# Kernel optimization log

Measured on AMD Instinct MI355X. Metric: run time of the kernel, lower is better.

Reference implementation:

```python
import jax, jax.numpy as jnp
from jax import lax
import numpy as np


def _lstm_dir(xg, w_hh, h0, c0, reverse):
    # xg: [B, L, 4H] precomputed input-gate contributions (incl. bias)
    def step(carry, xt):
        h, c = carry
        g = xt + h @ w_hh.T  # [B, 4H]
        i, f, gg, o = jnp.split(g, 4, axis=-1)  # torch gate order i,f,g,o
        c = jax.nn.sigmoid(f) * c + jax.nn.sigmoid(i) * jnp.tanh(gg)
        h = jax.nn.sigmoid(o) * jnp.tanh(c)
        return (h, c), h
    xs = jnp.swapaxes(xg, 0, 1)  # [L, B, 4H]
    _, hs = lax.scan(step, (h0, c0), xs, reverse=reverse)
    return jnp.swapaxes(hs, 0, 1)  # [B, L, H]


def _bilstm(x, w_ih_f, w_hh_f, b_f, w_ih_b, w_hh_b, b_b, h0, c0):
    B = x.shape[0]
    H = w_hh_f.shape[1]
    h0f = jnp.broadcast_to(h0[0], (B, H))
    c0f = jnp.broadcast_to(c0[0], (B, H))
    h0b = jnp.broadcast_to(h0[1], (B, H))
    c0b = jnp.broadcast_to(c0[1], (B, H))
    xg_f = jnp.einsum('bld,gd->blg', x, w_ih_f) + b_f
    xg_b = jnp.einsum('bld,gd->blg', x, w_ih_b) + b_b
    hf = _lstm_dir(xg_f, w_hh_f, h0f, c0f, False)
    hb = _lstm_dir(xg_b, w_hh_b, h0b, c0b, True)
    return jnp.concatenate([hf, hb], axis=-1)  # [B, L, 2H]


def _stem_forward(existence, unit_hidden, w_ih_f, w_hh_f, b_f, w_ih_b, w_hh_b, b_b,
                  orient_w, orient_b, h0, c0):
    ex = existence[..., None]                                  # [B, L, 1] bool
    uh = unit_hidden * ex.astype(unit_hidden.dtype)
    L = uh.shape[1]
    units, orients, exs = [], [], []
    for length in range(L, 0, -1):
        hs = _bilstm(uh, w_ih_f, w_hh_f, b_f, w_ih_b, w_hh_b, b_b, h0, c0)
        o = jnp.einsum('blh,oh->blo', hs, orient_w) + orient_b  # [B, length, 1]
        units.append(uh)
        orients.append(o)
        exs.append(ex)
        if length == 1:
            break
        right = o > 0
        lw = right[:, :-1] & ex[:, :-1]          # left child oriented right
        rw = (~right[:, 1:]) & ex[:, 1:]         # right child oriented left
        ex = lw | rw
        uh = uh[:, :-1] * lw.astype(uh.dtype) + uh[:, 1:] * rw.astype(uh.dtype)
    units.reverse(); orients.reverse(); exs.reverse()
    return (jnp.concatenate(units, axis=1),
            jnp.concatenate(orients, axis=1),
            jnp.concatenate(exs, axis=1))


def setup_inputs() -> dict:
    key = jax.random.key(0)
    ks = jax.random.split(key, 12)
    B, L, D, H = 128, 64, 512, 256
    s = 0.05
    return {
        'existence': jnp.ones((B, L), dtype=bool),
        'unit_hidden': jax.random.normal(ks[0], (B, L, D), jnp.float32),
        'w_ih_f': jax.random.normal(ks[1], (4 * H, D), jnp.float32) * s,
        'w_hh_f': jax.random.normal(ks[2], (4 * H, H), jnp.float32) * s,
        'b_f': jax.random.normal(ks[3], (4 * H,), jnp.float32) * s,
        'w_ih_b': jax.random.normal(ks[4], (4 * H, D), jnp.float32) * s,
        'w_hh_b': jax.random.normal(ks[5], (4 * H, H), jnp.float32) * s,
        'b_b': jax.random.normal(ks[6], (4 * H,), jnp.float32) * s,
        'orient_w': jax.random.normal(ks[7], (1, 2 * H), jnp.float32) * s,
        'orient_b': jax.random.normal(ks[8], (1,), jnp.float32) * s,
        'h0': jax.random.normal(ks[9], (2, 1, H), jnp.float32),
        'c0': jax.random.normal(ks[10], (2, 1, H), jnp.float32),
    }


def reference(existence, unit_hidden, w_ih_f, w_hh_f, b_f, w_ih_b, w_hh_b, b_b,
              orient_w, orient_b, h0, c0):
    return _stem_forward(existence, unit_hidden, w_ih_f, w_hh_f, b_f,
                         w_ih_b, w_hh_b, b_b, orient_w, orient_b, h0, c0)
```

## Files before the change

### kernel.cpp

```cpp
#include <hip/hip_runtime.h>
#include <cmath>

#define B 128
#define L 64
#define D 512
#define H 256
#define G4 1024
#define TOTROWS 2080
#define NBLK 256
#define GF_PAD 16

typedef float fx4 __attribute__((ext_vector_type(4)));

__device__ __forceinline__ float sigf(float x) { return 1.0f / (1.0f + expf(-x)); }

__device__ __forceinline__ void stg_sc_f32(float* p, float v) {
    asm volatile("global_store_dword %0, %1, off sc0 sc1" :: "v"(p), "v"(v) : "memory");
}
__device__ __forceinline__ void stg_sc_f64(double* p, double v) {
    asm volatile("global_store_dwordx2 %0, %1, off sc0 sc1" :: "v"(p), "v"(v) : "memory");
}
__device__ __forceinline__ void stg_sc_f4(float* p, float4 v) {
    fx4 w = __builtin_bit_cast(fx4, v);
    asm volatile("global_store_dwordx4 %0, %1, off sc0 sc1" :: "v"(p), "v"(w) : "memory");
}
__device__ __forceinline__ void ld4x4_sc(const float* p, fx4& a, fx4& b, fx4& c, fx4& d) {
    asm volatile(
        "global_load_dwordx4 %0, %4, off sc0 sc1\n\t"
        "global_load_dwordx4 %1, %4, off offset:16 sc0 sc1\n\t"
        "global_load_dwordx4 %2, %4, off offset:32 sc0 sc1\n\t"
        "global_load_dwordx4 %3, %4, off offset:48 sc0 sc1\n\t"
        "s_waitcnt vmcnt(0)"
        : "=&v"(a), "=&v"(b), "=&v"(c), "=&v"(d)
        : "v"(p) : "memory");
}
__device__ __forceinline__ bool any_nan(fx4 v) {
    return (v[0] != v[0]) | (v[1] != v[1]) | (v[2] != v[2]) | (v[3] != v[3]);
}

__device__ __forceinline__ void st_flag(int* p, int v) {
    __hip_atomic_store(p, v, __ATOMIC_RELAXED, __HIP_MEMORY_SCOPE_AGENT);
}
__device__ __forceinline__ int ld_flag(const int* p) {
    return __hip_atomic_load(p, __ATOMIC_RELAXED, __HIP_MEMORY_SCOPE_AGENT);
}

__device__ __forceinline__ void grid_barrier2(int* dflag, int* dgen, int bid, int phase) {
    __syncthreads();
    if (threadIdx.x == 0) {
        asm volatile("s_waitcnt vmcnt(0)" ::: "memory");
        st_flag(dflag + bid * GF_PAD, phase);
    }
    if (bid == 0) {
        if (threadIdx.x < 64) {
#pragma unroll
            for (int i = 0; i < 4; i++)
                while (ld_flag(dflag + (threadIdx.x * 4 + i) * GF_PAD) < phase)
                    __builtin_amdgcn_s_sleep(1);
        }
        __syncthreads();
        if (threadIdx.x == 0) st_flag(dgen, phase);
    } else if (threadIdx.x == 0) {
        while (ld_flag(dgen) < phase) __builtin_amdgcn_s_sleep(1);
    }
    __builtin_amdgcn_fence(__ATOMIC_ACQUIRE, "agent");
    __syncthreads();
}

__global__ __launch_bounds__(256) void k_init(const int* __restrict__ ex_in,
                                              const float* __restrict__ uh_in,
                                              float* __restrict__ units,
                                              float* __restrict__ exdst,
                                              float* __restrict__ hst,
                                              int* __restrict__ flags) {
    int idx = blockIdx.x * 256 + threadIdx.x;
    if (idx < 8192) flags[idx] = 0;
    {
        float qn = __uint_as_float(0x7fc00000u);
        float4 q4; q4.x = qn; q4.y = qn; q4.z = qn; q4.w = qn;
        ((float4*)hst)[idx] = q4;
    }
    int bt = idx >> 7;
    int r  = idx & 127;
    float m = (ex_in[bt] != 0) ? 1.0f : 0.0f;
    const float4* src = (const float4*)uh_in;
    float4 v = src[idx];
    v.x *= m; v.y *= m; v.z *= m; v.w *= m;
    int b = bt >> 6, t = bt & 63;
    float4* dst = (float4*)units;
    dst[((size_t)b * TOTROWS + 2016 + t) * 128 + r] = v;
    if (r == 0) exdst[bt] = m;
}

__global__ __launch_bounds__(256) void k_wprep_ih(const float* __restrict__ wf,
                                                  const float* __restrict__ wb,
                                                  float* __restrict__ wt) {
    int o = blockIdx.x * 256 + threadIdx.x;
    int n = o & 1023;
    int k = (o >> 10) & 511;
    int d = o >> 19;
    const float* W = d ? wb : wf;
    wt[o] = W[n * 512 + k];
}

__global__ __launch_bounds__(256) void k_wprep_hh(const float* __restrict__ wf,
                                                  const float* __restrict__ wb,
                                                  float* __restrict__ wt) {
    int o = blockIdx.x * 256 + threadIdx.x;
    int c    = o & 3;
    int i4   = (o >> 2) & 3;
    int q    = (o >> 4) & 3;
    int lane = (o >> 6) & 255;
    int jg   = (o >> 14) & 15;
    int d    = o >> 18;
    int jj = lane & 15, kseg = lane >> 4;
    const float* W = d ? wb : wf;
    wt[o] = W[(q * 256 + jg * 16 + jj) * 256 + kseg * 16 + i4 * 4 + c];
}

__global__ __launch_bounds__(256) void k_xg(const float* __restrict__ units,
                                            const float* __restrict__ wihT,
                                            float* __restrict__ xg, int len, int offL) {
    __shared__ __align__(16) float As[32 * 132];
    __shared__ __align__(16) float Bs[32 * 132];
    int tid = threadIdx.x;
    int nt = blockIdx.x, mtb = blockIdx.y;
    int d = nt >> 3;
    int gbase = (nt & 7) * 128;
    int M = 128 * len;

    int arow = tid & 127, ahalf = tid >> 7;
    int agm = mtb * 128 + arow;
    const float* aptr = nullptr;
    if (agm < M) {
        int ab = agm / len, at = agm - ab * len;
        aptr = units + ((size_t)ab * TOTROWS + offL + at) * 512;
    }
    int bcol = (tid & 31) * 4, bkr = tid >> 5;
    int tm = tid >> 4, tn = tid & 15;

    float acc[8][8];
#pragma unroll
    for (int i = 0; i < 8; i++)
#pragma unroll
        for (int j = 0; j < 8; j++) acc[i][j] = 0.f;

    for (int k0 = 0; k0 < 512; k0 += 32) {
#pragma unroll
        for (int i4 = 0; i4 < 4; i4++) {
            float4 v;
            if (aptr) v = *(const float4*)&aptr[k0 + ahalf * 16 + i4 * 4];
            else { v.x = v.y = v.z = v.w = 0.f; }
            int kk = ahalf * 16 + i4 * 4;
            As[(kk + 0) * 132 + arow] = v.x;
            As[(kk + 1) * 132 + arow] = v.y;
            As[(kk + 2) * 132 + arow] = v.z;
            As[(kk + 3) * 132 + arow] = v.w;
        }
#pragma unroll
        for (int i = 0; i < 4; i++) {
            int kk = bkr * 4 + i;
            float4 v = *(const float4*)&wihT[((size_t)(d * 512 + k0 + kk)) * 1024 + gbase + bcol];
            *(float4*)&Bs[kk * 132 + bcol] = v;
        }
        __syncthreads();
#pragma unroll 4
        for (int k = 0; k < 32; k++) {
            float4 a0 = *(const float4*)&As[k * 132 + tm * 8];
            float4 a1 = *(const float4*)&As[k * 132 + tm * 8 + 4];
            float4 b0 = *(const float4*)&Bs[k * 132 + tn * 8];
            float4 b1 = *(const float4*)&Bs[k * 132 + tn * 8 + 4];
            float av[8] = {a0.x, a0.y, a0.z, a0.w, a1.x, a1.y, a1.z, a1.w};
            float bv[8] = {b0.x, b0.y, b0.z, b0.w, b1.x, b1.y, b1.z, b1.w};
#pragma unroll
            for (int i = 0; i < 8; i++)
#pragma unroll
                for (int j = 0; j < 8; j++) acc[i][j] = fmaf(av[i], bv[j], acc[i][j]);
        }
        __syncthreads();
    }
#pragma unroll
    for (int i = 0; i < 8; i++) {
        int gm = mtb * 128 + tm * 8 + i;
        if (gm < M) {
            int bb = gm / len, tt = gm - bb * len;
            float* Cp = xg + ((size_t)(d * B + bb) * L + tt) * G4 + gbase + tn * 8;
            float4 v0; v0.x = acc[i][0]; v0.y = acc[i][1]; v0.z = acc[i][2]; v0.w = acc[i][3];
            float4 v1; v1.x = acc[i][4]; v1.y = acc[i][5]; v1.z = acc[i][6]; v1.w = acc[i][7];
            *(float4*)&Cp[0] = v0;
            *(float4*)&Cp[4] = v1;
        }
    }
}

__global__ __launch_bounds__(256, 1) void k_persist(
        float* __restrict__ xg, const float* __restrict__ wtHH,
        const float* __restrict__ bias_f, const float* __restrict__ bias_b,
        const float* __restrict__ ow, const float* __restrict__ h0,
        const float* __restrict__ c0, float* __restrict__ hst,
        double* __restrict__ o_part, const float* __restrict__ ob,
        float* __restrict__ exb0, float* __restrict__ exb1,
        float* __restrict__ dec, float* __restrict__ units,
        float* __restrict__ out_or, float* __restrict__ out_ex,
        int* flags) {
    __shared__ __align__(16) float hs[256 * 16];
    __shared__ __align__(16) float pb[8 * 16 * 68];
    __shared__ float osh[68];
    __shared__ float dsh[64];
    __shared__ float dsh2[64];
    int tid = threadIdx.x;
    int bid = blockIdx.x;
    int jg = bid & 15, sgd = bid >> 4;
    int sg = sgd & 7, d = sgd >> 3;
    int b0 = sg * 16, j0 = jg * 16;
    const size_t HB = (size_t)2 * B * H;

    int* dflag = flags;
    int* dgen  = flags + 4096;
    int dph = 0;

    float4 wreg[16];
    {
        const float4* wp = (const float4*)(wtHH + ((size_t)(d * 16 + jg) * 256 + tid) * 64);
#pragma unroll
        for (int m = 0; m < 16; m++) wreg[m] = wp[m];
    }
    int bF = tid >> 4, jjF = tid & 15;
    int bG = b0 + bF, jG = j0 + jjF;
    const float* biasp = d ? bias_b : bias_f;
    float bias4[4] = { biasp[jG], biasp[256 + jG], biasp[512 + jG], biasp[768 + jG] };
    float owv = ow[d * H + jG];
    float c0v = c0[d * H + jG];
    int bS = tid & 15, kc = tid >> 4;
    int swz = (((bS >> 2) ^ (kc & 3)) << 2) + (bS & 3);
    float4 h0s[4];
#pragma unroll
    for (int i4 = 0; i4 < 4; i4++)
        h0s[i4] = *(const float4*)&h0[d * H + kc * 16 + i4 * 4];
    const float* hstb = hst + ((size_t)(d * B + b0 + bS)) * H + kc * 16;
    float*       hwr  = hst + ((size_t)(d * B + bG)) * H + jG;
    float c_reg = 0.f;

    for (int it = 0; it < 64; ++it) {
        int len = 64 - it;
        int offL = len * (len - 1) / 2;
        int n = len - 1;
        const float* exs = (it & 1) ? exb1 : exb0;
        float* exd = (it & 1) ? exb0 : exb1;

        for (int s = 0; s < len; ++s) {
            int t = d ? (n - s) : s;
            size_t xgo = (((size_t)(d * B + bG)) * L + t) * G4 + jG;
            float x0 = xg[xgo], x1 = xg[xgo + 256], x2 = xg[xgo + 512], x3 = xg[xgo + 768];
            if (s == 0) {
#pragma unroll
                for (int i4 = 0; i4 < 4; i4++) {
                    int kk = kc * 16 + i4 * 4;
                    hs[(kk + 0) * 16 + swz] = h0s[i4].x;
                    hs[(kk + 1) * 16 + swz] = h0s[i4].y;
                    hs[(kk + 2) * 16 + swz] = h0s[i4].z;
                    hs[(kk + 3) * 16 + swz] = h0s[i4].w;
                }
            } else {
                const float* hp = hstb + (size_t)(s - 1) * HB;
                fx4 v0, v1, v2, v3;
                do { ld4x4_sc(hp, v0, v1, v2, v3); }
                while (any_nan(v0) | any_nan(v1) | any_nan(v2) | any_nan(v3));
                float arr[16] = { v0[0], v0[1], v0[2], v0[3], v1[0], v1[1], v1[2], v1[3],
                                  v2[0], v2[1], v2[2], v2[3], v3[0], v3[1], v3[2], v3[3] };
#pragma unroll
                for (int i = 0; i < 16; i++)
                    hs[(kc * 16 + i) * 16 + swz] = arr[i];
            }
            __syncthreads();
            {
                int jj = tid & 15, kseg = tid >> 4;
                int ks3 = kseg & 3;
                float acc[4][16];
#pragma unroll
                for (int q = 0; q < 4; q++)
#pragma unroll
                    for (int u = 0; u < 16; u++) acc[q][u] = 0.f;
#pragma unroll
                for (int i4 = 0; i4 < 4; i4++) {
#pragma unroll
                    for (int c = 0; c < 4; c++) {
                        int k = (kseg << 4) + (i4 << 2) + c;
                        const float* hb = &hs[k << 4];
                        float4 hv[4];
#pragma unroll
                        for (int bq = 0; bq < 4; bq++)
                            hv[bq] = *(const float4*)&hb[((bq ^ ks3) << 2)];
#pragma unroll
                        for (int q = 0; q < 4; q++) {
                            float4 wv = wreg[q * 4 + i4];
                            float w = (c == 0) ? wv.x : (c == 1) ? wv.y : (c == 2) ? wv.z : wv.w;
#pragma unroll
                            for (int bq = 0; bq < 4; bq++) {
                                acc[q][bq * 4 + 0] = fmaf(hv[bq].x, w, acc[q][bq * 4 + 0]);
                                acc[q][bq * 4 + 1] = fmaf(hv[bq].y, w, acc[q][bq * 4 + 1]);
                                acc[q][bq * 4 + 2] = fmaf(hv[bq].z, w, acc[q][bq * 4 + 2]);
                                acc[q][bq * 4 + 3] = fmaf(hv[bq].w, w, acc[q][bq * 4 + 3]);
                            }
                        }
                    }
                }
#pragma unroll
                for (int q = 0; q < 4; q++)
#pragma unroll
                    for (int u = 0; u < 16; u++) acc[q][u] += __shfl_xor(acc[q][u], 32);
                if (!(tid & 32)) {
                    int slice = ((tid >> 6) << 1) | ((tid >> 4) & 1);
                    float* pbp = &pb[(slice * 16 + jj) * 68];
#pragma unroll
                    for (int bb = 0; bb < 16; bb++) {
                        float4 v; v.x = acc[0][bb]; v.y = acc[1][bb]; v.z = acc[2][bb]; v.w = acc[3][bb];
                        *(float4*)&pbp[bb * 4] = v;
                    }
                }
            }
            __syncthreads();
            {
                float g4[4] = {0.f, 0.f, 0.f, 0.f};
#pragma unroll
                for (int sl = 0; sl < 8; sl++) {
                    float4 pv = *(const float4*)&pb[(sl * 16 + jjF) * 68 + bF * 4];
                    g4[0] += pv.x; g4[1] += pv.y; g4[2] += pv.z; g4[3] += pv.w;
                }
                float g0 = x0 + bias4[0] + g4[0];
                float g1 = x1 + bias4[1] + g4[1];
                float g2 = x2 + bias4[2] + g4[2];
                float g3 = x3 + bias4[3] + g4[3];
                float c_old = (s == 0) ? c0v : c_reg;
                float ig = sigf(g0);
                float fg = sigf(g1);
                float gv = tanhf(g2);
                float og = sigf(g3);
                float c = fg * c_old + ig * gv;
                float h = og * tanhf(c);
                c_reg = c;
                stg_sc_f32(hwr + (size_t)s * HB, h);
                double contrib = (double)h * (double)owv;
#pragma unroll
                for (int off = 8; off > 0; off >>= 1) contrib += __shfl_xor(contrib, off, 16);
                if (jjF == 0) stg_sc_f64(&o_part[(((size_t)(d * 16 + jg)) * B + bG) * L + t], contrib);
            }
            __syncthreads();
        }
        ++dph; grid_barrier2(dflag, dgen, bid, dph);

        if (bid < 128) {
            int b = bid;
            float oval = 0.f, exval = 0.f;
            if (tid < len) {
                double sum = (double)ob[0];
#pragma unroll 4
                for (int i = 0; i < 32; i++) sum += o_part[((size_t)i * B + b) * L + tid];
                oval = (float)sum;
                osh[tid] = oval;
                exval = exs[b * L + tid];
                stg_sc_f32(out_or + (size_t)b * TOTROWS + offL + tid, oval);
                stg_sc_f32(out_ex + (size_t)b * TOTROWS + offL + tid, exval);
            }
            __syncthreads();
            if (tid < len - 1) {
                float on  = osh[tid + 1];
                float exn = exs[b * L + tid + 1];
                float lw = (oval > 0.f && exval != 0.f) ? 1.f : 0.f;
                float rw = (!(on > 0.f) && exn != 0.f) ? 1.f : 0.f;
                stg_sc_f32(dec + b * L + tid, lw + 2.f * rw);
                stg_sc_f32(exd + b * L + tid, ((lw + rw) > 0.f) ? 1.f : 0.f);
            }
        }
        ++dph; grid_barrier2(dflag, dgen, bid, dph);

        if (len > 1) {
            int bu = bid >> 1;
            int b2 = bid & 127;
            if (tid < n) dsh[tid]  = dec[bu * L + tid];
            if (tid < n) dsh2[tid] = dec[b2 * L + tid];
            __syncthreads();
            {
                int k = ((bid & 1) << 8) + tid;
                const float* src = units + ((size_t)bu * TOTROWS + offL) * D + k;
                float* dst = units + ((size_t)bu * TOTROWS + (offL - n)) * D + k;
                float cur = src[0];
                int tt = 0;
                while (tt < n) {
                    int m = (n - tt < 8) ? (n - tt) : 8;
                    float nx[8];
#pragma unroll
                    for (int i = 0; i < 8; i++) if (i < m) nx[i] = src[(size_t)(tt + i + 1) * D];
#pragma unroll
                    for (int i = 0; i < 8; i++) if (i < m) {
                        int dv = (int)dsh[tt + i];
                        stg_sc_f32(dst + (size_t)(tt + i) * D,
                                   (float)(dv & 1) * cur + (float)(dv >> 1) * nx[i]);
                        cur = nx[i];
                    }
                    tt += m;
                }
            }
            {
                int d2 = bid >> 7;
                float* base = xg + ((size_t)(d2 * B + b2) * L) * G4 + tid * 4;
                float4 cur = *(const float4*)base;
                int tt = 0;
                while (tt < n) {
                    int m = (n - tt < 8) ? (n - tt) : 8;
                    float4 nx[8];
#pragma unroll
                    for (int i = 0; i < 8; i++) if (i < m)
                        nx[i] = *(const float4*)(base + (size_t)(tt + i + 1) * G4);
#pragma unroll
                    for (int i = 0; i < 8; i++) if (i < m) {
                        int dv = (int)dsh2[tt + i];
                        float flw = (float)(dv & 1), frw = (float)(dv >> 1);
                        float4 o;
                        o.x = flw * cur.x + frw * nx[i].x;
                        o.y = flw * cur.y + frw * nx[i].y;
                        o.z = flw * cur.z + frw * nx[i].z;
                        o.w = flw * cur.w + frw * nx[i].w;
                        stg_sc_f4(base + (size_t)(tt + i) * G4, o);
                        cur = nx[i];
                    }
                    tt += m;
                }
            }
            {
                float qn = __uint_as_float(0x7fc00000u);
                for (int s2 = 0; s2 < n; ++s2)
                    stg_sc_f32(hwr + (size_t)s2 * HB, qn);
            }
            ++dph; grid_barrier2(dflag, dgen, bid, dph);
        }
    }
}

extern "C" void kernel_launch(void* const* d_in, const int* in_sizes, int n_in,
                              void* d_out, int out_size, void* d_ws, size_t ws_size,
                              hipStream_t stream) {
    const int*   ex_in   = (const int*)d_in[0];
    const float* uh_in   = (const float*)d_in[1];
    const float* w_ih_f  = (const float*)d_in[2];
    const float* w_hh_f  = (const float*)d_in[3];
    const float* b_f     = (const float*)d_in[4];
    const float* w_ih_b  = (const float*)d_in[5];
    const float* w_hh_b  = (const float*)d_in[6];
    const float* b_b     = (const float*)d_in[7];
    const float* orientw = (const float*)d_in[8];
    const float* orientb = (const float*)d_in[9];
    const float* h0      = (const float*)d_in[10];
    const float* c0      = (const float*)d_in[11];

    float* units  = (float*)d_out;
    float* out_or = units + (size_t)B * TOTROWS * D;
    float* out_ex = out_or + (size_t)B * TOTROWS;

    float* xg    = (float*)d_ws;
    float* wihT  = xg + (size_t)2 * B * L * G4;
    float* wtHH  = wihT + (size_t)1048576;
    float* hst   = wtHH + (size_t)524288;
    float* dec   = hst + (size_t)64 * 2 * B * H;
    float* exb0  = dec + B * L;
    float* exb1  = exb0 + B * L;
    double* opart = (double*)(exb1 + B * L);
    int*   flags = (int*)(opart + 262144);

    k_init<<<4096, 256, 0, stream>>>(ex_in, uh_in, units, exb0, hst, flags);
    k_wprep_ih<<<4096, 256, 0, stream>>>(w_ih_f, w_ih_b, wihT);
    k_wprep_hh<<<2048, 256, 0, stream>>>(w_hh_f, w_hh_b, wtHH);
    k_xg<<<dim3(16, 64), 256, 0, stream>>>(units, wihT, xg, 64, 2016);
    k_persist<<<NBLK, 256, 0, stream>>>(xg, wtHH, b_f, b_b, orientw, h0, c0,
                                        hst, opart, orientb,
                                        exb0, exb1, dec, units, out_or, out_ex, flags);
    (void)in_sizes; (void)n_in; (void)out_size; (void)ws_size;
}
```

Measured before the change: 12.90 ms.

## Replace NaN-sentinel polling of hidden state with per-group step counters

Blocks used to spin-reload the 64-byte h slice until it contained no NaNs, which required NaN-filling the whole hst buffer at init and re-poisoning it after every outer iteration. Each writer now publishes a monotonically increasing step tag per (batch row, column group) after a vmcnt wait, and readers poll that single int before loading h once. This removes the NaN init and re-poison stores but adds a full store drain and an extra flag store on every step.

```diff
diff --git a/kernel.cpp b/kernel.cpp
--- a/kernel.cpp
+++ b/kernel.cpp
@@ -23,6 +23,15 @@
 __device__ __forceinline__ void stg_sc_f4(float* p, float4 v) {
     fx4 w = __builtin_bit_cast(fx4, v);
     asm volatile("global_store_dwordx4 %0, %1, off sc0 sc1" :: "v"(p), "v"(w) : "memory");
+}
+__device__ __forceinline__ void stg_sc_u32(int* p, int v) {
+    asm volatile("global_store_dword %0, %1, off sc0 sc1" :: "v"(p), "v"(v) : "memory");
+}
+__device__ __forceinline__ int ld_sc_u32(const int* p) {
+    int v;
+    asm volatile("global_load_dword %0, %1, off sc0 sc1\n\ts_waitcnt vmcnt(0)"
+                 : "=v"(v) : "v"(p) : "memory");
+    return v;
 }
 __device__ __forceinline__ void ld4x4_sc(const float* p, fx4& a, fx4& b, fx4& c, fx4& d) {
     asm volatile(
@@ -34,9 +43,6 @@
         : "=&v"(a), "=&v"(b), "=&v"(c), "=&v"(d)
         : "v"(p) : "memory");
 }
-__device__ __forceinline__ bool any_nan(fx4 v) {
-    return (v[0] != v[0]) | (v[1] != v[1]) | (v[2] != v[2]) | (v[3] != v[3]);
-}
 
 __device__ __forceinline__ void st_flag(int* p, int v) {
     __hip_atomic_store(p, v, __ATOMIC_RELAXED, __HIP_MEMORY_SCOPE_AGENT);
@@ -71,15 +77,9 @@
                                               const float* __restrict__ uh_in,
                                               float* __restrict__ units,
                                               float* __restrict__ exdst,
-                                              float* __restrict__ hst,
                                               int* __restrict__ flags) {
     int idx = blockIdx.x * 256 + threadIdx.x;
-    if (idx < 8192) flags[idx] = 0;
-    {
-        float qn = __uint_as_float(0x7fc00000u);
-        float4 q4; q4.x = qn; q4.y = qn; q4.z = qn; q4.w = qn;
-        ((float4*)hst)[idx] = q4;
-    }
+    if (idx < 8448) flags[idx] = 0;
     int bt = idx >> 7;
     int r  = idx & 127;
     float m = (ex_in[bt] != 0) ? 1.0f : 0.0f;
@@ -217,7 +217,9 @@
 
     int* dflag = flags;
     int* dgen  = flags + 4096;
+    int* sents = flags + 4352;
     int dph = 0;
+    int T0 = 0;
 
     float4 wreg[16];
     {
@@ -239,6 +241,8 @@
         h0s[i4] = *(const float4*)&h0[d * H + kc * 16 + i4 * 4];
     const float* hstb = hst + ((size_t)(d * B + b0 + bS)) * H + kc * 16;
     float*       hwr  = hst + ((size_t)(d * B + bG)) * H + jG;
+    int* sent_wr = sents + sgd * 256 + jg * 16 + bF;
+    int* sent_rd = sents + sgd * 256 + kc * 16 + bS;
     float c_reg = 0.f;
 
     for (int it = 0; it < 64; ++it) {
@@ -262,10 +266,11 @@
                     hs[(kk + 3) * 16 + swz] = h0s[i4].w;
                 }
             } else {
+                int tag = T0 + s;
+                while (ld_sc_u32(sent_rd) < tag) __builtin_amdgcn_s_sleep(1);
                 const float* hp = hstb + (size_t)(s - 1) * HB;
                 fx4 v0, v1, v2, v3;
-                do { ld4x4_sc(hp, v0, v1, v2, v3); }
-                while (any_nan(v0) | any_nan(v1) | any_nan(v2) | any_nan(v3));
+                ld4x4_sc(hp, v0, v1, v2, v3);
                 float arr[16] = { v0[0], v0[1], v0[2], v0[3], v1[0], v1[1], v1[2], v1[3],
                                   v2[0], v2[1], v2[2], v2[3], v3[0], v3[1], v3[2], v3[3] };
 #pragma unroll
@@ -344,6 +349,8 @@
 #pragma unroll
                 for (int off = 8; off > 0; off >>= 1) contrib += __shfl_xor(contrib, off, 16);
                 if (jjF == 0) stg_sc_f64(&o_part[(((size_t)(d * 16 + jg)) * B + bG) * L + t], contrib);
+                asm volatile("s_waitcnt vmcnt(0)" ::: "memory");
+                if (jjF == 0) stg_sc_u32(sent_wr, T0 + s + 1);
             }
             __syncthreads();
         }
@@ -427,13 +434,9 @@
                     tt += m;
                 }
             }
-            {
-                float qn = __uint_as_float(0x7fc00000u);
-                for (int s2 = 0; s2 < n; ++s2)
-                    stg_sc_f32(hwr + (size_t)s2 * HB, qn);
-            }
             ++dph; grid_barrier2(dflag, dgen, bid, dph);
         }
+        T0 += len;
     }
 }
 
@@ -467,7 +470,7 @@
     double* opart = (double*)(exb1 + B * L);
     int*   flags = (int*)(opart + 262144);
 
-    k_init<<<4096, 256, 0, stream>>>(ex_in, uh_in, units, exb0, hst, flags);
+    k_init<<<4096, 256, 0, stream>>>(ex_in, uh_in, units, exb0, flags);
     k_wprep_ih<<<4096, 256, 0, stream>>>(w_ih_f, w_ih_b, wihT);
     k_wprep_hh<<<2048, 256, 0, stream>>>(w_hh_f, w_hh_b, wtHH);
     k_xg<<<dim3(16, 64), 256, 0, stream>>>(units, wihT, xg, 64, 2016);
```

After: 14.61 ms. +13.2%, slower.

## Halve persistent grid, process two batch groups per block, drop a grid barrier

Applied to the files above, without the earlier changes.

The persistent LSTM kernel now runs on 128 blocks instead of 256. Each block handles two 16-row batch groups in sequence per timestep and keeps twice as many K-slices per thread, so the partial-sum reduction has fewer slices. Per-batch existence and decision state now stay in shared memory inside the block that owns that batch, which removes the global dec/ex buffers and one grid-wide barrier per level. The cost is more serial work per block on each recurrent step, and there may be less overlap across CUs.

```diff
diff --git a/kernel.cpp b/kernel.cpp
--- a/kernel.cpp
+++ b/kernel.cpp
@@ -7,7 +7,7 @@
 #define H 256
 #define G4 1024
 #define TOTROWS 2080
-#define NBLK 256
+#define NBLK 128
 #define GF_PAD 16
 
 typedef float fx4 __attribute__((ext_vector_type(4)));
@@ -54,8 +54,8 @@
     if (bid == 0) {
         if (threadIdx.x < 64) {
 #pragma unroll
-            for (int i = 0; i < 4; i++)
-                while (ld_flag(dflag + (threadIdx.x * 4 + i) * GF_PAD) < phase)
+            for (int i = 0; i < 2; i++)
+                while (ld_flag(dflag + (threadIdx.x * 2 + i) * GF_PAD) < phase)
                     __builtin_amdgcn_s_sleep(1);
         }
         __syncthreads();
@@ -70,11 +70,10 @@
 __global__ __launch_bounds__(256) void k_init(const int* __restrict__ ex_in,
                                               const float* __restrict__ uh_in,
                                               float* __restrict__ units,
-                                              float* __restrict__ exdst,
                                               float* __restrict__ hst,
                                               int* __restrict__ flags) {
     int idx = blockIdx.x * 256 + threadIdx.x;
-    if (idx < 8192) flags[idx] = 0;
+    if (idx < 8448) flags[idx] = 0;
     {
         float qn = __uint_as_float(0x7fc00000u);
         float4 q4; q4.x = qn; q4.y = qn; q4.z = qn; q4.w = qn;
@@ -89,7 +88,6 @@
     int b = bt >> 6, t = bt & 63;
     float4* dst = (float4*)units;
     dst[((size_t)b * TOTROWS + 2016 + t) * 128 + r] = v;
-    if (r == 0) exdst[bt] = m;
 }
 
 __global__ __launch_bounds__(256) void k_wprep_ih(const float* __restrict__ wf,
@@ -199,20 +197,20 @@
         const float* __restrict__ ow, const float* __restrict__ h0,
         const float* __restrict__ c0, float* __restrict__ hst,
         double* __restrict__ o_part, const float* __restrict__ ob,
-        float* __restrict__ exb0, float* __restrict__ exb1,
-        float* __restrict__ dec, float* __restrict__ units,
+        const int* __restrict__ ex_in, float* __restrict__ units,
         float* __restrict__ out_or, float* __restrict__ out_ex,
         int* flags) {
-    __shared__ __align__(16) float hs[256 * 16];
-    __shared__ __align__(16) float pb[8 * 16 * 68];
+    __shared__ __align__(16) float hsA[256 * 16];
+    __shared__ __align__(16) float hsB[256 * 16];
+    __shared__ __align__(16) float pb[4 * 16 * 68];
     __shared__ float osh[68];
     __shared__ float dsh[64];
-    __shared__ float dsh2[64];
+    __shared__ float exl[64];
     int tid = threadIdx.x;
     int bid = blockIdx.x;
-    int jg = bid & 15, sgd = bid >> 4;
-    int sg = sgd & 7, d = sgd >> 3;
-    int b0 = sg * 16, j0 = jg * 16;
+    int jg = bid & 15, sgp = (bid >> 4) & 3, d = bid >> 6;
+    int j0 = jg * 16;
+    int b0A = sgp * 32, b0B = sgp * 32 + 16;
     const size_t HB = (size_t)2 * B * H;
 
     int* dflag = flags;
@@ -226,7 +224,8 @@
         for (int m = 0; m < 16; m++) wreg[m] = wp[m];
     }
     int bF = tid >> 4, jjF = tid & 15;
-    int bG = b0 + bF, jG = j0 + jjF;
+    int jG = j0 + jjF;
+    int bGA = b0A + bF, bGB = b0B + bF;
     const float* biasp = d ? bias_b : bias_f;
     float bias4[4] = { biasp[jG], biasp[256 + jG], biasp[512 + jG], biasp[768 + jG] };
     float owv = ow[d * H + jG];
@@ -237,173 +236,169 @@
 #pragma unroll
     for (int i4 = 0; i4 < 4; i4++)
         h0s[i4] = *(const float4*)&h0[d * H + kc * 16 + i4 * 4];
-    const float* hstb = hst + ((size_t)(d * B + b0 + bS)) * H + kc * 16;
-    float*       hwr  = hst + ((size_t)(d * B + bG)) * H + jG;
-    float c_reg = 0.f;
+    const float* hstbA = hst + ((size_t)(d * B + b0A + bS)) * H + kc * 16;
+    const float* hstbB = hst + ((size_t)(d * B + b0B + bS)) * H + kc * 16;
+    float* hwrA = hst + ((size_t)(d * B + bGA)) * H + jG;
+    float* hwrB = hst + ((size_t)(d * B + bGB)) * H + jG;
+    float c_regA = 0.f, c_regB = 0.f;
+    if (tid < 64) exl[tid] = (ex_in[bid * 64 + tid] != 0) ? 1.0f : 0.0f;
+
+#define CHAIN_PHASE(HS, HSTB, HWR, BG, CREG)                                         \
+    {                                                                                \
+        size_t xgo = (((size_t)(d * B + (BG))) * L + t) * G4 + jG;                   \
+        float x0 = xg[xgo], x1 = xg[xgo + 256];                                      \
+        float x2 = xg[xgo + 512], x3 = xg[xgo + 768];                                \
+        if (s == 0) {                                                                \
+            for (int i4 = 0; i4 < 4; i4++) {                                         \
+                int kk = kc * 16 + i4 * 4;                                           \
+                HS[(kk + 0) * 16 + swz] = h0s[i4].x;                                 \
+                HS[(kk + 1) * 16 + swz] = h0s[i4].y;                                 \
+                HS[(kk + 2) * 16 + swz] = h0s[i4].z;                                 \
+                HS[(kk + 3) * 16 + swz] = h0s[i4].w;                                 \
+            }                                                                        \
+        } else {                                                                     \
+            const float* hp = (HSTB) + (size_t)(s - 1) * HB;                         \
+            fx4 v0, v1, v2, v3;                                                      \
+            ld4x4_sc(hp, v0, v1, v2, v3);                                            \
+            while (any_nan(v0) | any_nan(v1) | any_nan(v2) | any_nan(v3)) {          \
+                __builtin_amdgcn_s_sleep(2);                                         \
+                ld4x4_sc(hp, v0, v1, v2, v3);                                        \
+            }                                                                        \
+            float arr[16] = { v0[0], v0[1], v0[2], v0[3], v1[0], v1[1], v1[2], v1[3],\
+                              v2[0], v2[1], v2[2], v2[3], v3[0], v3[1], v3[2], v3[3] };\
+            for (int i = 0; i < 16; i++)                                             \
+                HS[(kc * 16 + i) * 16 + swz] = arr[i];                               \
+        }                                                                            \
+        __syncthreads();                                                             \
+        {                                                                            \
+            int jj = tid & 15, kseg = tid >> 4;                                      \
+            int ks3 = kseg & 3;                                                      \
+            float acc[4][16];                                                        \
+            for (int q = 0; q < 4; q++)                                              \
+                for (int u = 0; u < 16; u++) acc[q][u] = 0.f;                        \
+            for (int i4 = 0; i4 < 4; i4++) {                                         \
+                for (int c = 0; c < 4; c++) {                                        \
+                    int k = (kseg << 4) + (i4 << 2) + c;                             \
+                    const float* hb = &HS[k << 4];                                   \
+                    float4 hv[4];                                                    \
+                    for (int bq = 0; bq < 4; bq++)                                   \
+                        hv[bq] = *(const float4*)&hb[((bq ^ ks3) << 2)];             \
+                    for (int q = 0; q < 4; q++) {                                    \
+                        float4 wv = wreg[q * 4 + i4];                                \
+                        float w = (c == 0) ? wv.x : (c == 1) ? wv.y                  \
+                                 : (c == 2) ? wv.z : wv.w;                           \
+                        for (int bq = 0; bq < 4; bq++) {                             \
+                            acc[q][bq * 4 + 0] = fmaf(hv[bq].x, w, acc[q][bq * 4 + 0]);\
+                            acc[q][bq * 4 + 1] = fmaf(hv[bq].y, w, acc[q][bq * 4 + 1]);\
+                            acc[q][bq * 4 + 2] = fmaf(hv[bq].z, w, acc[q][bq * 4 + 2]);\
+                            acc[q][bq * 4 + 3] = fmaf(hv[bq].w, w, acc[q][bq * 4 + 3]);\
+                        }                                                            \
+                    }                                                                \
+                }                                                                    \
+            }                                                                        \
+            for (int q = 0; q < 4; q++)                                              \
+                for (int u = 0; u < 16; u++) {                                       \
+                    acc[q][u] += __shfl_xor(acc[q][u], 16);                          \
+                    acc[q][u] += __shfl_xor(acc[q][u], 32);                          \
+                }                                                                    \
+            if (!(tid & 48)) {                                                       \
+                int slice = tid >> 6;                                                \
+                float* pbp = &pb[(slice * 16 + jj) * 68];                            \
+                for (int bb = 0; bb < 16; bb++) {                                    \
+                    float4 v; v.x = acc[0][bb]; v.y = acc[1][bb];                    \
+                    v.z = acc[2][bb]; v.w = acc[3][bb];                              \
+                    *(float4*)&pbp[bb * 4] = v;                                      \
+                }                                                                    \
+            }                                                                        \
+        }                                                                            \
+        __syncthreads();                                                             \
+        {                                                                            \
+            float g4[4] = {0.f, 0.f, 0.f, 0.f};                                      \
+            for (int sl = 0; sl < 4; sl++) {                                         \
+                float4 pv = *(const float4*)&pb[(sl * 16 + jjF) * 68 + bF * 4];      \
+                g4[0] += pv.x; g4[1] += pv.y; g4[2] += pv.z; g4[3] += pv.w;          \
+            }                                                                        \
+            float g0 = x0 + bias4[0] + g4[0];                                        \
+            float g1 = x1 + bias4[1] + g4[1];                                        \
+            float g2 = x2 + bias4[2] + g4[2];                                        \
+            float g3 = x3 + bias4[3] + g4[3];                                        \
+            float c_old = (s == 0) ? c0v : (CREG);                                   \
+            float ig = sigf(g0);                                                     \
+            float fg = sigf(g1);                                                     \
+            float gv = tanhf(g2);                                                    \
+            float og = sigf(g3);                                                     \
+            float cc = fg * c_old + ig * gv;                                         \
+            float hh = og * tanhf(cc);                                               \
+            (CREG) = cc;                                                             \
+            stg_sc_f32((HWR) + (size_t)s * HB, hh);                                  \
+            double contrib = (double)hh * (double)owv;                               \
+            for (int off = 8; off > 0; off >>= 1)                                    \
+                contrib += __shfl_xor(contrib, off, 16);                             \
+            if (jjF == 0)                                                            \
+                stg_sc_f64(&o_part[(((size_t)(d * 16 + jg)) * B + (BG)) * L + t], contrib);\
+        }                                                                            \
+    }
 
     for (int it = 0; it < 64; ++it) {
         int len = 64 - it;
         int offL = len * (len - 1) / 2;
         int n = len - 1;
-        const float* exs = (it & 1) ? exb1 : exb0;
-        float* exd = (it & 1) ? exb0 : exb1;
 
         for (int s = 0; s < len; ++s) {
             int t = d ? (n - s) : s;
-            size_t xgo = (((size_t)(d * B + bG)) * L + t) * G4 + jG;
-            float x0 = xg[xgo], x1 = xg[xgo + 256], x2 = xg[xgo + 512], x3 = xg[xgo + 768];
-            if (s == 0) {
-#pragma unroll
-                for (int i4 = 0; i4 < 4; i4++) {
-                    int kk = kc * 16 + i4 * 4;
-                    hs[(kk + 0) * 16 + swz] = h0s[i4].x;
-                    hs[(kk + 1) * 16 + swz] = h0s[i4].y;
-                    hs[(kk + 2) * 16 + swz] = h0s[i4].z;
-                    hs[(kk + 3) * 16 + swz] = h0s[i4].w;
-                }
-            } else {
-                const float* hp = hstb + (size_t)(s - 1) * HB;
-                fx4 v0, v1, v2, v3;
-                do { ld4x4_sc(hp, v0, v1, v2, v3); }
-                while (any_nan(v0) | any_nan(v1) | any_nan(v2) | any_nan(v3));
-                float arr[16] = { v0[0], v0[1], v0[2], v0[3], v1[0], v1[1], v1[2], v1[3],
-                                  v2[0], v2[1], v2[2], v2[3], v3[0], v3[1], v3[2], v3[3] };
-#pragma unroll
-                for (int i = 0; i < 16; i++)
-                    hs[(kc * 16 + i) * 16 + swz] = arr[i];
-            }
-            __syncthreads();
-            {
-                int jj = tid & 15, kseg = tid >> 4;
-                int ks3 = kseg & 3;
-                float acc[4][16];
-#pragma unroll
-                for (int q = 0; q < 4; q++)
-#pragma unroll
-                    for (int u = 0; u < 16; u++) acc[q][u] = 0.f;
-#pragma unroll
-                for (int i4 = 0; i4 < 4; i4++) {
-#pragma unroll
-                    for (int c = 0; c < 4; c++) {
-                        int k = (kseg << 4) + (i4 << 2) + c;
-                        const float* hb = &hs[k << 4];
-                        float4 hv[4];
-#pragma unroll
-                        for (int bq = 0; bq < 4; bq++)
-                            hv[bq] = *(const float4*)&hb[((bq ^ ks3) << 2)];
-#pragma unroll
-                        for (int q = 0; q < 4; q++) {
-                            float4 wv = wreg[q * 4 + i4];
-                            float w = (c == 0) ? wv.x : (c == 1) ? wv.y : (c == 2) ? wv.z : wv.w;
-#pragma unroll
-                            for (int bq = 0; bq < 4; bq++) {
-                                acc[q][bq * 4 + 0] = fmaf(hv[bq].x, w, acc[q][bq * 4 + 0]);
-                                acc[q][bq * 4 + 1] = fmaf(hv[bq].y, w, acc[q][bq * 4 + 1]);
-                                acc[q][bq * 4 + 2] = fmaf(hv[bq].z, w, acc[q][bq * 4 + 2]);
-                                acc[q][bq * 4 + 3] = fmaf(hv[bq].w, w, acc[q][bq * 4 + 3]);
-                            }
-                        }
-                    }
-                }
-#pragma unroll
-                for (int q = 0; q < 4; q++)
-#pragma unroll
-                    for (int u = 0; u < 16; u++) acc[q][u] += __shfl_xor(acc[q][u], 32);
-                if (!(tid & 32)) {
-                    int slice = ((tid >> 6) << 1) | ((tid >> 4) & 1);
-                    float* pbp = &pb[(slice * 16 + jj) * 68];
-#pragma unroll
-                    for (int bb = 0; bb < 16; bb++) {
-                        float4 v; v.x = acc[0][bb]; v.y = acc[1][bb]; v.z = acc[2][bb]; v.w = acc[3][bb];
-                        *(float4*)&pbp[bb * 4] = v;
-                    }
-                }
-            }
-            __syncthreads();
-            {
-                float g4[4] = {0.f, 0.f, 0.f, 0.f};
-#pragma unroll
-                for (int sl = 0; sl < 8; sl++) {
-                    float4 pv = *(const float4*)&pb[(sl * 16 + jjF) * 68 + bF * 4];
-                    g4[0] += pv.x; g4[1] += pv.y; g4[2] += pv.z; g4[3] += pv.w;
-                }
-                float g0 = x0 + bias4[0] + g4[0];
-                float g1 = x1 + bias4[1] + g4[1];
-                float g2 = x2 + bias4[2] + g4[2];
-                float g3 = x3 + bias4[3] + g4[3];
-                float c_old = (s == 0) ? c0v : c_reg;
-                float ig = sigf(g0);
-                float fg = sigf(g1);
-                float gv = tanhf(g2);
-                float og = sigf(g3);
-                float c = fg * c_old + ig * gv;
-                float h = og * tanhf(c);
-                c_reg = c;
-                stg_sc_f32(hwr + (size_t)s * HB, h);
-                double contrib = (double)h * (double)owv;
-#pragma unroll
-                for (int off = 8; off > 0; off >>= 1) contrib += __shfl_xor(contrib, off, 16);
-                if (jjF == 0) stg_sc_f64(&o_part[(((size_t)(d * 16 + jg)) * B + bG) * L + t], contrib);
-            }
-            __syncthreads();
+            CHAIN_PHASE(hsA, hstbA, hwrA, bGA, c_regA)
+            CHAIN_PHASE(hsB, hstbB, hwrB, bGB, c_regB)
         }
         ++dph; grid_barrier2(dflag, dgen, bid, dph);
 
-        if (bid < 128) {
+        {
             int b = bid;
-            float oval = 0.f, exval = 0.f;
+            float oval = 0.f;
             if (tid < len) {
                 double sum = (double)ob[0];
 #pragma unroll 4
                 for (int i = 0; i < 32; i++) sum += o_part[((size_t)i * B + b) * L + tid];
                 oval = (float)sum;
                 osh[tid] = oval;
-                exval = exs[b * L + tid];
-                stg_sc_f32(out_or + (size_t)b * TOTROWS + offL + tid, oval);
-                stg_sc_f32(out_ex + (size_t)b * TOTROWS + offL + tid, exval);
+                out_or[(size_t)b * TOTROWS + offL + tid] = oval;
+                out_ex[(size_t)b * TOTROWS + offL + tid] = exl[tid];
             }
             __syncthreads();
-            if (tid < len - 1) {
-                float on  = osh[tid + 1];
-                float exn = exs[b * L + tid + 1];
-                float lw = (oval > 0.f && exval != 0.f) ? 1.f : 0.f;
-                float rw = (!(on > 0.f) && exn != 0.f) ? 1.f : 0.f;
-                stg_sc_f32(dec + b * L + tid, lw + 2.f * rw);
-                stg_sc_f32(exd + b * L + tid, ((lw + rw) > 0.f) ? 1.f : 0.f);
+            if (tid < n) {
+                float lw = (oval > 0.f && exl[tid] != 0.f) ? 1.f : 0.f;
+                float rw = (!(osh[tid + 1] > 0.f) && exl[tid + 1] != 0.f) ? 1.f : 0.f;
+                dsh[tid] = lw + 2.f * rw;
             }
-        }
-        ++dph; grid_barrier2(dflag, dgen, bid, dph);
+            __syncthreads();
+            if (tid < n) exl[tid] = (dsh[tid] != 0.f) ? 1.f : 0.f;
+            __syncthreads();
+        }
 
         if (len > 1) {
-            int bu = bid >> 1;
-            int b2 = bid & 127;
-            if (tid < n) dsh[tid]  = dec[bu * L + tid];
-            if (tid < n) dsh2[tid] = dec[b2 * L + tid];
-            __syncthreads();
-            {
-                int k = ((bid & 1) << 8) + tid;
-                const float* src = units + ((size_t)bu * TOTROWS + offL) * D + k;
-                float* dst = units + ((size_t)bu * TOTROWS + (offL - n)) * D + k;
-                float cur = src[0];
+            int b = bid;
+#pragma unroll
+            for (int kk2 = 0; kk2 < 2; ++kk2) {
+                int k = kk2 * 256 + tid;
+                const float* srcp = units + ((size_t)b * TOTROWS + offL) * D + k;
+                float* dstp = units + ((size_t)b * TOTROWS + (offL - n)) * D + k;
+                float cur = srcp[0];
                 int tt = 0;
                 while (tt < n) {
                     int m = (n - tt < 8) ? (n - tt) : 8;
                     float nx[8];
 #pragma unroll
-                    for (int i = 0; i < 8; i++) if (i < m) nx[i] = src[(size_t)(tt + i + 1) * D];
+                    for (int i = 0; i < 8; i++) if (i < m) nx[i] = srcp[(size_t)(tt + i + 1) * D];
 #pragma unroll
                     for (int i = 0; i < 8; i++) if (i < m) {
                         int dv = (int)dsh[tt + i];
-                        stg_sc_f32(dst + (size_t)(tt + i) * D,
-                                   (float)(dv & 1) * cur + (float)(dv >> 1) * nx[i]);
+                        dstp[(size_t)(tt + i) * D] = (float)(dv & 1) * cur + (float)(dv >> 1) * nx[i];
                         cur = nx[i];
                     }
                     tt += m;
                 }
             }
-            {
-                int d2 = bid >> 7;
-                float* base = xg + ((size_t)(d2 * B + b2) * L) * G4 + tid * 4;
+            for (int d2 = 0; d2 < 2; ++d2) {
+                float* base = xg + ((size_t)(d2 * B + b) * L) * G4 + tid * 4;
                 float4 cur = *(const float4*)base;
                 int tt = 0;
                 while (tt < n) {
@@ -414,7 +409,7 @@
                         nx[i] = *(const float4*)(base + (size_t)(tt + i + 1) * G4);
 #pragma unroll
                     for (int i = 0; i < 8; i++) if (i < m) {
-                        int dv = (int)dsh2[tt + i];
+                        int dv = (int)dsh[tt + i];
                         float flw = (float)(dv & 1), frw = (float)(dv >> 1);
                         float4 o;
                         o.x = flw * cur.x + frw * nx[i].x;
@@ -429,12 +424,15 @@
             }
             {
                 float qn = __uint_as_float(0x7fc00000u);
-                for (int s2 = 0; s2 < n; ++s2)
-                    stg_sc_f32(hwr + (size_t)s2 * HB, qn);
+                for (int s2 = 0; s2 < n; ++s2) {
+                    stg_sc_f32(hwrA + (size_t)s2 * HB, qn);
+                    stg_sc_f32(hwrB + (size_t)s2 * HB, qn);
+                }
             }
             ++dph; grid_barrier2(dflag, dgen, bid, dph);
         }
     }
+#undef CHAIN_PHASE
 }
 
 extern "C" void kernel_launch(void* const* d_in, const int* in_sizes, int n_in,
@@ -461,18 +459,15 @@
     float* wihT  = xg + (size_t)2 * B * L * G4;
     float* wtHH  = wihT + (size_t)1048576;
     float* hst   = wtHH + (size_t)524288;
-    float* dec   = hst + (size_t)64 * 2 * B * H;
-    float* exb0  = dec + B * L;
-    float* exb1  = exb0 + B * L;
-    double* opart = (double*)(exb1 + B * L);
+    double* opart = (double*)(hst + (size_t)64 * 2 * B * H);
     int*   flags = (int*)(opart + 262144);
 
-    k_init<<<4096, 256, 0, stream>>>(ex_in, uh_in, units, exb0, hst, flags);
+    k_init<<<4096, 256, 0, stream>>>(ex_in, uh_in, units, hst, flags);
     k_wprep_ih<<<4096, 256, 0, stream>>>(w_ih_f, w_ih_b, wihT);
     k_wprep_hh<<<2048, 256, 0, stream>>>(w_hh_f, w_hh_b, wtHH);
     k_xg<<<dim3(16, 64), 256, 0, stream>>>(units, wihT, xg, 64, 2016);
     k_persist<<<NBLK, 256, 0, stream>>>(xg, wtHH, b_f, b_b, orientw, h0, c0,
-                                        hst, opart, orientb,
-                                        exb0, exb1, dec, units, out_or, out_ex, flags);
+                                        hst, opart, orientb, ex_in,
+                                        units, out_or, out_ex, flags);
     (void)in_sizes; (void)n_in; (void)out_size; (void)ws_size;
 }
```

New measurement: 23.29 ms. +80.5%, slower.

## Replace grid-wide barriers with per-batch-group barriers and keep existence in LDS

Applied to the files above, without the earlier changes.

Swaps the full 256-block grid barrier for independent barriers across the 32 blocks that share a 16-batch slice, since later work only depends on data within that slice. The per-length decision and compaction work is remapped so each group handles its own batches, and the existence mask now lives in shared memory instead of global ping-pong buffers. A small sleep is added to the NaN-poll spin loop. This cuts cross-device synchronisation latency and lets groups drift apart, but it relies on the o_part partials and dec writes being confined to a group, which a mistake in the index remapping would break.

```diff
diff --git a/kernel.cpp b/kernel.cpp
--- a/kernel.cpp
+++ b/kernel.cpp
@@ -45,23 +45,17 @@
     return __hip_atomic_load(p, __ATOMIC_RELAXED, __HIP_MEMORY_SCOPE_AGENT);
 }
 
-__device__ __forceinline__ void grid_barrier2(int* dflag, int* dgen, int bid, int phase) {
+__device__ __forceinline__ void group_barrier(int* gflag, int* ggen, int lid, int phase) {
+    asm volatile("s_waitcnt vmcnt(0)" ::: "memory");
     __syncthreads();
-    if (threadIdx.x == 0) {
-        asm volatile("s_waitcnt vmcnt(0)" ::: "memory");
-        st_flag(dflag + bid * GF_PAD, phase);
-    }
-    if (bid == 0) {
-        if (threadIdx.x < 64) {
-#pragma unroll
-            for (int i = 0; i < 4; i++)
-                while (ld_flag(dflag + (threadIdx.x * 4 + i) * GF_PAD) < phase)
-                    __builtin_amdgcn_s_sleep(1);
-        }
+    if (threadIdx.x == 0) st_flag(gflag + lid * GF_PAD, phase);
+    if (lid == 0) {
+        if (threadIdx.x < 32)
+            while (ld_flag(gflag + threadIdx.x * GF_PAD) < phase) __builtin_amdgcn_s_sleep(1);
         __syncthreads();
-        if (threadIdx.x == 0) st_flag(dgen, phase);
+        if (threadIdx.x == 0) st_flag(ggen, phase);
     } else if (threadIdx.x == 0) {
-        while (ld_flag(dgen) < phase) __builtin_amdgcn_s_sleep(1);
+        while (ld_flag(ggen) < phase) __builtin_amdgcn_s_sleep(1);
     }
     __builtin_amdgcn_fence(__ATOMIC_ACQUIRE, "agent");
     __syncthreads();
@@ -70,11 +64,10 @@
 __global__ __launch_bounds__(256) void k_init(const int* __restrict__ ex_in,
                                               const float* __restrict__ uh_in,
                                               float* __restrict__ units,
-                                              float* __restrict__ exdst,
                                               float* __restrict__ hst,
                                               int* __restrict__ flags) {
     int idx = blockIdx.x * 256 + threadIdx.x;
-    if (idx < 8192) flags[idx] = 0;
+    if (idx < 8448) flags[idx] = 0;
     {
         float qn = __uint_as_float(0x7fc00000u);
         float4 q4; q4.x = qn; q4.y = qn; q4.z = qn; q4.w = qn;
@@ -89,7 +82,6 @@
     int b = bt >> 6, t = bt & 63;
     float4* dst = (float4*)units;
     dst[((size_t)b * TOTROWS + 2016 + t) * 128 + r] = v;
-    if (r == 0) exdst[bt] = m;
 }
 
 __global__ __launch_bounds__(256) void k_wprep_ih(const float* __restrict__ wf,
@@ -199,25 +191,24 @@
         const float* __restrict__ ow, const float* __restrict__ h0,
         const float* __restrict__ c0, float* __restrict__ hst,
         double* __restrict__ o_part, const float* __restrict__ ob,
-        float* __restrict__ exb0, float* __restrict__ exb1,
-        float* __restrict__ dec, float* __restrict__ units,
-        float* __restrict__ out_or, float* __restrict__ out_ex,
-        int* flags) {
+        const int* __restrict__ ex_in, float* __restrict__ dec,
+        float* __restrict__ units, float* __restrict__ out_or,
+        float* __restrict__ out_ex, int* flags) {
     __shared__ __align__(16) float hs[256 * 16];
     __shared__ __align__(16) float pb[8 * 16 * 68];
     __shared__ float osh[68];
     __shared__ float dsh[64];
-    __shared__ float dsh2[64];
+    __shared__ float exl[64];
     int tid = threadIdx.x;
     int bid = blockIdx.x;
-    int jg = bid & 15, sgd = bid >> 4;
-    int sg = sgd & 7, d = sgd >> 3;
+    int jg = bid & 15, sg = (bid >> 4) & 7, d = bid >> 7;
+    int lid = jg + 16 * d;
     int b0 = sg * 16, j0 = jg * 16;
     const size_t HB = (size_t)2 * B * H;
 
-    int* dflag = flags;
-    int* dgen  = flags + 4096;
-    int dph = 0;
+    int* gflag = flags + sg * 32 * GF_PAD;
+    int* ggen  = flags + 4096 + sg * GF_PAD;
+    int gph = 0;
 
     float4 wreg[16];
     {
@@ -240,13 +231,12 @@
     const float* hstb = hst + ((size_t)(d * B + b0 + bS)) * H + kc * 16;
     float*       hwr  = hst + ((size_t)(d * B + bG)) * H + jG;
     float c_reg = 0.f;
+    if (d == 0 && tid < 64) exl[tid] = (ex_in[(b0 + jg) * 64 + tid] != 0) ? 1.0f : 0.0f;
 
     for (int it = 0; it < 64; ++it) {
         int len = 64 - it;
         int offL = len * (len - 1) / 2;
         int n = len - 1;
-        const float* exs = (it & 1) ? exb1 : exb0;
-        float* exd = (it & 1) ? exb0 : exb1;
 
         for (int s = 0; s < len; ++s) {
             int t = d ? (n - s) : s;
@@ -264,8 +254,11 @@
             } else {
                 const float* hp = hstb + (size_t)(s - 1) * HB;
                 fx4 v0, v1, v2, v3;
-                do { ld4x4_sc(hp, v0, v1, v2, v3); }
-                while (any_nan(v0) | any_nan(v1) | any_nan(v2) | any_nan(v3));
+                ld4x4_sc(hp, v0, v1, v2, v3);
+                while (any_nan(v0) | any_nan(v1) | any_nan(v2) | any_nan(v3)) {
+                    __builtin_amdgcn_s_sleep(2);
+                    ld4x4_sc(hp, v0, v1, v2, v3);
+                }
                 float arr[16] = { v0[0], v0[1], v0[2], v0[3], v1[0], v1[1], v1[2], v1[3],
                                   v2[0], v2[1], v2[2], v2[3], v3[0], v3[1], v3[2], v3[3] };
 #pragma unroll
@@ -347,41 +340,39 @@
             }
             __syncthreads();
         }
-        ++dph; grid_barrier2(dflag, dgen, bid, dph);
-
-        if (bid < 128) {
-            int b = bid;
-            float oval = 0.f, exval = 0.f;
+        ++gph; group_barrier(gflag, ggen, lid, gph);
+
+        if (d == 0) {
+            int bo = b0 + jg;
+            float oval = 0.f;
             if (tid < len) {
                 double sum = (double)ob[0];
 #pragma unroll 4
-                for (int i = 0; i < 32; i++) sum += o_part[((size_t)i * B + b) * L + tid];
+                for (int i = 0; i < 32; i++) sum += o_part[((size_t)i * B + bo) * L + tid];
                 oval = (float)sum;
                 osh[tid] = oval;
-                exval = exs[b * L + tid];
-                stg_sc_f32(out_or + (size_t)b * TOTROWS + offL + tid, oval);
-                stg_sc_f32(out_ex + (size_t)b * TOTROWS + offL + tid, exval);
-            }
-            __syncthreads();
-            if (tid < len - 1) {
-                float on  = osh[tid + 1];
-                float exn = exs[b * L + tid + 1];
-                float lw = (oval > 0.f && exval != 0.f) ? 1.f : 0.f;
-                float rw = (!(on > 0.f) && exn != 0.f) ? 1.f : 0.f;
-                stg_sc_f32(dec + b * L + tid, lw + 2.f * rw);
-                stg_sc_f32(exd + b * L + tid, ((lw + rw) > 0.f) ? 1.f : 0.f);
-            }
-        }
-        ++dph; grid_barrier2(dflag, dgen, bid, dph);
+                out_or[(size_t)bo * TOTROWS + offL + tid] = oval;
+                out_ex[(size_t)bo * TOTROWS + offL + tid] = exl[tid];
+            }
+            __syncthreads();
+            float newex = 0.f;
+            if (tid < n) {
+                float lw = (oval > 0.f && exl[tid] != 0.f) ? 1.f : 0.f;
+                float rw = (!(osh[tid + 1] > 0.f) && exl[tid + 1] != 0.f) ? 1.f : 0.f;
+                stg_sc_f32(dec + bo * 64 + tid, lw + 2.f * rw);
+                newex = ((lw + rw) > 0.f) ? 1.f : 0.f;
+            }
+            __syncthreads();
+            if (tid < n) exl[tid] = newex;
+        }
+        ++gph; group_barrier(gflag, ggen, lid, gph);
 
         if (len > 1) {
-            int bu = bid >> 1;
-            int b2 = bid & 127;
-            if (tid < n) dsh[tid]  = dec[bu * L + tid];
-            if (tid < n) dsh2[tid] = dec[b2 * L + tid];
+            int bu = b0 + (lid >> 1);
+            if (tid < n) dsh[tid] = dec[bu * 64 + tid];
             __syncthreads();
             {
-                int k = ((bid & 1) << 8) + tid;
+                int k = ((lid & 1) << 8) + tid;
                 const float* src = units + ((size_t)bu * TOTROWS + offL) * D + k;
                 float* dst = units + ((size_t)bu * TOTROWS + (offL - n)) * D + k;
                 float cur = src[0];
@@ -402,8 +393,8 @@
                 }
             }
             {
-                int d2 = bid >> 7;
-                float* base = xg + ((size_t)(d2 * B + b2) * L) * G4 + tid * 4;
+                int d2 = lid & 1;
+                float* base = xg + ((size_t)(d2 * B + bu) * L) * G4 + tid * 4;
                 float4 cur = *(const float4*)base;
                 int tt = 0;
                 while (tt < n) {
@@ -414,7 +405,7 @@
                         nx[i] = *(const float4*)(base + (size_t)(tt + i + 1) * G4);
 #pragma unroll
                     for (int i = 0; i < 8; i++) if (i < m) {
-                        int dv = (int)dsh2[tt + i];
+                        int dv = (int)dsh[tt + i];
                         float flw = (float)(dv & 1), frw = (float)(dv >> 1);
                         float4 o;
                         o.x = flw * cur.x + frw * nx[i].x;
@@ -432,7 +423,7 @@
                 for (int s2 = 0; s2 < n; ++s2)
                     stg_sc_f32(hwr + (size_t)s2 * HB, qn);
             }
-            ++dph; grid_barrier2(dflag, dgen, bid, dph);
+            ++gph; group_barrier(gflag, ggen, lid, gph);
         }
     }
 }
@@ -462,17 +453,15 @@
     float* wtHH  = wihT + (size_t)1048576;
     float* hst   = wtHH + (size_t)524288;
     float* dec   = hst + (size_t)64 * 2 * B * H;
-    float* exb0  = dec + B * L;
-    float* exb1  = exb0 + B * L;
-    double* opart = (double*)(exb1 + B * L);
+    double* opart = (double*)(dec + B * L);
     int*   flags = (int*)(opart + 262144);
 
-    k_init<<<4096, 256, 0, stream>>>(ex_in, uh_in, units, exb0, hst, flags);
+    k_init<<<4096, 256, 0, stream>>>(ex_in, uh_in, units, hst, flags);
     k_wprep_ih<<<4096, 256, 0, stream>>>(w_ih_f, w_ih_b, wihT);
     k_wprep_hh<<<2048, 256, 0, stream>>>(w_hh_f, w_hh_b, wtHH);
     k_xg<<<dim3(16, 64), 256, 0, stream>>>(units, wihT, xg, 64, 2016);
     k_persist<<<NBLK, 256, 0, stream>>>(xg, wtHH, b_f, b_b, orientw, h0, c0,
-                                        hst, opart, orientb,
-                                        exb0, exb1, dec, units, out_or, out_ex, flags);
+                                        hst, opart, orientb, ex_in, dec,
+                                        units, out_or, out_ex, flags);
     (void)in_sizes; (void)n_in; (void)out_size; (void)ws_size;
 }
```

Measured after the change: 11.77 ms. 1.1x faster.
